# Kernel optimization log

Hardware: AMD Instinct MI355X
Metric: run time of the kernel (lower is better)

The kernel has to match this reference:

```python
import jax, jax.numpy as jnp
from jax import lax
import numpy as np

# ---- static config (matches init_kwargs) ----
B, H, W = 8, 32, 32
L = H * W                      # 1024 tokens
D_MODEL = 384
MAMBA_DIM = 192                # d_model * d_mamba_ratio
LOCAL_DIM = 192
D_INNER = 384                  # expand_m * MAMBA_DIM
D_STATE = 16
D_CONV = 4
DT_RANK = 12                   # ceil(MAMBA_DIM / 16)
NDIR = 4                       # h, h_flip, v, v_flip
RED = 48                       # int(D_INNER * 0.125), BiAttn reduce dim
INNER_C = 192                  # LOCAL_DIM * expand_c
K_C = 8                        # local block depthwise kernel size


def setup_inputs() -> dict:
    key = jax.random.key(0)
    ks = jax.random.split(key, 16)
    s = 0.02
    return {
        "x": jax.random.normal(ks[0], (B, L, D_MODEL), jnp.float32),
        "in_proj_w": jax.random.normal(ks[1], (2 * D_INNER, MAMBA_DIM)) * s,
        "A_log": jnp.broadcast_to(jnp.log(jnp.arange(1, D_STATE + 1, dtype=jnp.float32)), (NDIR, D_INNER, D_STATE)) + 0.0,
        "conv_w": jax.random.normal(ks[2], (NDIR, D_INNER, D_CONV)) * 0.2,
        "conv_b": jax.random.normal(ks[3], (NDIR, D_INNER)) * 0.02,
        "xproj_w": jax.random.normal(ks[4], (NDIR, DT_RANK + 2 * D_STATE, D_INNER)) * s,
        "dtproj_w": jax.random.normal(ks[5], (NDIR, D_INNER, DT_RANK)) * (DT_RANK ** -0.5),
        "dtproj_b": jax.random.normal(ks[6], (NDIR, D_INNER)) * 0.5 - 4.0,
        "Dp": jnp.ones((NDIR, D_INNER)),
        "out_proj_w": jax.random.normal(ks[7], (MAMBA_DIM, D_INNER)) * s,
        "attn_ln_g": jnp.ones((D_INNER,)),
        "attn_ln_b": jnp.zeros((D_INNER,)),
        "attn_gr_w": jax.random.normal(ks[8], (RED, D_INNER)) * s,
        "attn_gr_b": jnp.zeros((RED,)),
        "attn_cs_w": jax.random.normal(ks[9], (D_INNER, RED)) * s,
        "attn_cs_b": jnp.zeros((D_INNER,)),
        "pw1_w": jax.random.normal(ks[10], (2 * INNER_C, LOCAL_DIM)) * s,
        "pw1_b": jnp.zeros((2 * INNER_C,)),
        "dw_w": jax.random.normal(ks[11], (INNER_C, K_C)) * 0.2,
        "dw_b": jnp.zeros((INNER_C,)),
        "bn_g": jnp.ones((INNER_C,)),
        "bn_b": jnp.zeros((INNER_C,)),
        "pw2_w": jax.random.normal(ks[12], (LOCAL_DIM, INNER_C)) * s,
        "pw2_b": jnp.zeros((LOCAL_DIM,)),
    }


def _forward(x, in_proj_w, A_log, conv_w, conv_b, xproj_w, dtproj_w, dtproj_b, Dp,
             out_proj_w, attn_ln_g, attn_ln_b, attn_gr_w, attn_gr_b, attn_cs_w, attn_cs_b,
             pw1_w, pw1_b, dw_w, dw_b, bn_g, bn_b, pw2_w, pw2_b):
    mamba_in = x[:, :, :MAMBA_DIM]
    local_in = x[:, :, MAMBA_DIM:]

    # ---------- MultiMamba branch ----------
    xz = jnp.swapaxes(mamba_in @ in_proj_w.T, 1, 2)   # (B, 2*D_INNER, L)

    def to_dir(t, i):
        # reorder channel-last-token axis per scan direction
        if i == 0:
            return t
        if i == 1:
            return jnp.flip(t, -1)
        tv = t.reshape(B, -1, H, W).swapaxes(-1, -2).reshape(B, -1, L)  # column-major scan
        return tv if i == 2 else jnp.flip(tv, -1)

    def from_dir(t, i):
        if i == 0:
            return t
        if i == 1:
            return jnp.flip(t, -1)
        if i == 3:
            t = jnp.flip(t, -1)
        return t.reshape(B, -1, W, H).swapaxes(-1, -2).reshape(B, -1, L)

    def ssm_dir(xzd, i):
        # mamba_inner_fn_no_out_proj: causal dwconv -> silu -> x_proj -> selective scan -> gate
        xp, z = jnp.split(xzd, 2, axis=1)            # (B, D_INNER, L) each
        xpad = jnp.pad(xp, ((0, 0), (0, 0), (D_CONV - 1, 0)))
        u = lax.conv_general_dilated(xpad, conv_w[i][:, None, :], (1,), 'VALID',
                                     dimension_numbers=('NCH', 'OIH', 'NCH'),
                                     feature_group_count=D_INNER)
        u = jax.nn.silu(u + conv_b[i][None, :, None])
        dbl = jnp.einsum('bdl,rd->brl', u, xproj_w[i])
        dt = dbl[:, :DT_RANK]
        Bm = dbl[:, DT_RANK:DT_RANK + D_STATE]
        Cm = dbl[:, DT_RANK + D_STATE:]
        delta = jax.nn.softplus(jnp.einsum('brl,dr->bdl', dt, dtproj_w[i]) + dtproj_b[i][None, :, None])
        A = -jnp.exp(A_log[i])                        # (D_INNER, D_STATE)

        def step(h, inps):
            d_t, B_t, C_t, u_t = inps                 # (B,d),(B,n),(B,n),(B,d)
            h = jnp.exp(d_t[:, :, None] * A) * h + (d_t * u_t)[:, :, None] * B_t[:, None, :]
            return h, jnp.einsum('bdn,bn->bd', h, C_t)

        h0 = jnp.zeros((B, D_INNER, D_STATE), x.dtype)
        _, ys = lax.scan(step, h0, (delta.transpose(2, 0, 1), Bm.transpose(2, 0, 1),
                                    Cm.transpose(2, 0, 1), u.transpose(2, 0, 1)))
        y = ys.transpose(1, 2, 0) + u * Dp[i][:, None]  # (B, D_INNER, L)
        return y * jax.nn.silu(z)

    def biattn(t):                                     # (B, L, D_INNER)
        mu = t.mean(-1, keepdims=True)
        var = ((t - mu) ** 2).mean(-1, keepdims=True)
        tn = (t - mu) / jnp.sqrt(var + 1e-5) * attn_ln_g + attn_ln_b
        g = tn.mean(1, keepdims=True)                  # global pool (B,1,D_INNER)
        g = jax.nn.gelu(g @ attn_gr_w.T + attn_gr_b, approximate=False)
        c = jax.nn.sigmoid(g @ attn_cs_w.T + attn_cs_b)
        return t * c

    acc = jnp.zeros((B, L, D_INNER), x.dtype)
    for i in range(NDIR):                              # fixed small set of directions
        out_i = from_dir(ssm_dir(to_dir(xz, i), i), i)
        acc = acc + biattn(jnp.swapaxes(out_i, 1, 2))
    mamba_out = acc @ out_proj_w.T                     # (B, L, MAMBA_DIM)

    # ---------- Local conv branch ----------
    hch = jnp.einsum('blc,oc->bol', local_in, pw1_w) + pw1_b[None, :, None]
    a, gte = jnp.split(hch, 2, axis=1)
    hch = a * jax.nn.sigmoid(gte)                      # GLU, (B, INNER_C, L)
    pad_l = K_C // 2
    pad_r = K_C // 2 - (K_C + 1) % 2                   # calc_same_padding(8) -> (4, 3)
    hpad = jnp.pad(hch, ((0, 0), (0, 0), (pad_l, pad_r)))
    hch = lax.conv_general_dilated(hpad, dw_w[:, None, :], (1,), 'VALID',
                                   dimension_numbers=('NCH', 'OIH', 'NCH'),
                                   feature_group_count=INNER_C) + dw_b[None, :, None]
    mu = hch.mean((0, 2))                              # BatchNorm1d (training-mode batch stats)
    var = hch.var((0, 2))
    hch = (hch - mu[None, :, None]) / jnp.sqrt(var + 1e-5)[None, :, None] * bn_g[None, :, None] + bn_b[None, :, None]
    hch = hch * jax.nn.sigmoid(hch)                    # Swish
    local_out = jnp.einsum('bcl,oc->blo', hch, pw2_w) + pw2_b

    return jnp.concatenate([mamba_out, local_out], axis=-1)


def reference(x, in_proj_w, A_log, conv_w, conv_b, xproj_w, dtproj_w, dtproj_b, Dp,
              out_proj_w, attn_ln_g, attn_ln_b, attn_gr_w, attn_gr_b, attn_cs_w, attn_cs_b,
              pw1_w, pw1_b, dw_w, dw_b, bn_g, bn_b, pw2_w, pw2_b):
    return _forward(x, in_proj_w, A_log, conv_w, conv_b, xproj_w, dtproj_w, dtproj_b, Dp,
                    out_proj_w, attn_ln_g, attn_ln_b, attn_gr_w, attn_gr_b, attn_cs_w, attn_cs_b,
                    pw1_w, pw1_b, dw_w, dw_b, bn_g, bn_b, pw2_w, pw2_b)
```

## Files before the change

### kernel.cpp

```cpp
#include <hip/hip_runtime.h>
#include <stdint.h>


#define DEV __device__ __forceinline__

typedef __attribute__((ext_vector_type(8))) short short8;
typedef __attribute__((ext_vector_type(4))) short short4v;
typedef __attribute__((ext_vector_type(4))) float f32x4;

DEV float bf(ushort v) { union { uint32_t u; float f; } c; c.u = ((uint32_t)v) << 16; return c.f; }
DEV ushort fbf(float f) {
  union { float f; uint32_t u; } c; c.f = f;
  uint32_t u = c.u;
  return (ushort)((u + 0x7FFFu + ((u >> 16) & 1u)) >> 16);
}

#if __has_builtin(__builtin_amdgcn_exp2f)
DEV float fexp2(float x) { return __builtin_amdgcn_exp2f(x); }
#else
DEV float fexp2(float x) { return __expf(x * 0.6931471805599453f); }
#endif

template<int CTRL>
DEV float rradd(float x) {
  return x + __int_as_float(__builtin_amdgcn_update_dpp(
      0, __float_as_int(x), CTRL, 0xF, 0xF, true));
}

DEV int pmap(int i, int j) {
  if (i == 0) return j;
  if (i == 1) return 1023 - j;
  if (i == 2) return ((j & 31) << 5) | (j >> 5);
  int k = 1023 - j; return ((k & 31) << 5) | (k >> 5);
}

DEV void cvt4(const float* __restrict__ s, ushort* __restrict__ d, int blk, int tid) {
  const int idx = (blk * 256 + tid) * 4;
  float4 v = *(const float4*)(s + idx);
  d[idx] = fbf(v.x); d[idx + 1] = fbf(v.y); d[idx + 2] = fbf(v.z); d[idx + 3] = fbf(v.w);
}

__global__ __launch_bounds__(256) void prep_all(
    const float* __restrict__ x, ushort* __restrict__ xb,
    const float* __restrict__ ipw, ushort* __restrict__ ipwb,
    const float* __restrict__ opw, ushort* __restrict__ opwb,
    const float* __restrict__ pw1w, ushort* __restrict__ pw1wb,
    const float* __restrict__ pw2w, ushort* __restrict__ pw2wb,
    const float* __restrict__ xw, ushort* __restrict__ xwp)
{
  const int bx = blockIdx.x, tid = threadIdx.x;
  if (bx < 3072)      cvt4(x, xb, bx, tid);
  else if (bx < 3216) cvt4(ipw, ipwb, bx - 3072, tid);
  else if (bx < 3288) cvt4(opw, opwb, bx - 3216, tid);
  else if (bx < 3360) cvt4(pw1w, pw1wb, bx - 3288, tid);
  else if (bx < 3396) cvt4(pw2w, pw2wb, bx - 3360, tid);
  else {
    const int row = bx - 3396;
    const int i = row >> 6, nn = row & 63;
    for (int c = tid; c < 384; c += 256)
      xwp[(size_t)row * 384 + c] = (nn < 44) ? fbf(xw[((size_t)i * 44 + nn) * 384 + c]) : (ushort)0;
  }
}

template<bool BF16OUT, bool BIAS>
__global__ __launch_bounds__(256) void gemm_bt(
    const ushort* __restrict__ A, long long sAz, int lda,
    const ushort* __restrict__ Bw, long long sBz,
    const float* __restrict__ bias,
    void* __restrict__ C, long long sCz, int ldc, int coff, int K)
{
  __shared__ ushort As[64][40];
  __shared__ ushort Bs[64][40];
  A += (size_t)blockIdx.z * sAz;
  Bw += (size_t)blockIdx.z * sBz;
  const int tid = threadIdx.x;
  const int m0 = blockIdx.x * 64, n0 = blockIdx.y * 64;
  const int w = tid >> 6, lane = tid & 63, l15 = lane & 15, quad = lane >> 4;
  const int sr = tid >> 2, sc = (tid & 3) * 8;
  f32x4 acc[4] = {};
  for (int k0 = 0; k0 < K; k0 += 32) {
    __syncthreads();
    *(short8*)&As[sr][sc] = *(const short8*)(A + (size_t)(m0 + sr) * lda + k0 + sc);
    *(short8*)&Bs[sr][sc] = *(const short8*)(Bw + (size_t)(n0 + sr) * K + k0 + sc);
    __syncthreads();
    short8 av = *(short8*)&As[w * 16 + l15][quad * 8];
#pragma unroll
    for (int nt = 0; nt < 4; nt++) {
      short8 bv = *(short8*)&Bs[nt * 16 + l15][quad * 8];
      acc[nt] = __builtin_amdgcn_mfma_f32_16x16x32_bf16(av, bv, acc[nt], 0, 0, 0);
    }
  }
  float* cf = (float*)C + (size_t)blockIdx.z * sCz;
  ushort* cb = (ushort*)C + (size_t)blockIdx.z * sCz;
#pragma unroll
  for (int nt = 0; nt < 4; nt++) {
    const int col = n0 + nt * 16 + l15;
    const float bv = BIAS ? bias[col] : 0.f;
#pragma unroll
    for (int r = 0; r < 4; r++) {
      const int row = m0 + w * 16 + quad * 4 + r;
      float v = acc[nt][r] + bv;
      if (BF16OUT) cb[(size_t)row * ldc + coff + col] = fbf(v);
      else         cf[(size_t)row * ldc + coff + col] = v;
    }
  }
}

__global__ __launch_bounds__(256) void gemm_dual(
    const ushort* __restrict__ A0, int lda0, const ushort* __restrict__ B0,
    const float* __restrict__ bias0, void* __restrict__ C0, int ldc0, int coff0, int K0,
    int nt0, int bf0,
    const ushort* __restrict__ A1, int lda1, const ushort* __restrict__ B1,
    const float* __restrict__ bias1, void* __restrict__ C1, int ldc1, int coff1, int K1,
    int bf1)
{
  __shared__ ushort As[64][40];
  __shared__ ushort Bs[64][40];
  const ushort* A; const ushort* Bw; const float* bias; void* C;
  int lda, ldc, coff, K, bf16o, n0;
  if ((int)blockIdx.y < nt0) {
    A = A0; lda = lda0; Bw = B0; bias = bias0; C = C0; ldc = ldc0; coff = coff0; K = K0;
    bf16o = bf0; n0 = blockIdx.y * 64;
  } else {
    A = A1; lda = lda1; Bw = B1; bias = bias1; C = C1; ldc = ldc1; coff = coff1; K = K1;
    bf16o = bf1; n0 = (blockIdx.y - nt0) * 64;
  }
  const int tid = threadIdx.x;
  const int m0 = blockIdx.x * 64;
  const int w = tid >> 6, lane = tid & 63, l15 = lane & 15, quad = lane >> 4;
  const int sr = tid >> 2, sc = (tid & 3) * 8;
  f32x4 acc[4] = {};
  for (int k0 = 0; k0 < K; k0 += 32) {
    __syncthreads();
    *(short8*)&As[sr][sc] = *(const short8*)(A + (size_t)(m0 + sr) * lda + k0 + sc);
    *(short8*)&Bs[sr][sc] = *(const short8*)(Bw + (size_t)(n0 + sr) * K + k0 + sc);
    __syncthreads();
    short8 av = *(short8*)&As[w * 16 + l15][quad * 8];
#pragma unroll
    for (int nt = 0; nt < 4; nt++) {
      short8 bv = *(short8*)&Bs[nt * 16 + l15][quad * 8];
      acc[nt] = __builtin_amdgcn_mfma_f32_16x16x32_bf16(av, bv, acc[nt], 0, 0, 0);
    }
  }
#pragma unroll
  for (int nt = 0; nt < 4; nt++) {
    const int col = n0 + nt * 16 + l15;
    const float bv = bias ? bias[col] : 0.f;
#pragma unroll
    for (int r = 0; r < 4; r++) {
      const int row = m0 + w * 16 + quad * 4 + r;
      float v = acc[nt][r] + bv;
      if (bf16o) ((ushort*)C)[(size_t)row * ldc + coff + col] = fbf(v);
      else       ((float*)C)[(size_t)row * ldc + coff + col] = v;
    }
  }
}

__global__ __launch_bounds__(256) void gemm_pw2(
    const float* __restrict__ h2, const float* __restrict__ bnsum,
    const float* __restrict__ bng, const float* __restrict__ bnb,
    const ushort* __restrict__ Bw, const float* __restrict__ bias,
    float* __restrict__ C)
{
  __shared__ ushort As[64][40];
  __shared__ ushort Bs[64][40];
  __shared__ float bsc[192], bsh[192];
  const int tid = threadIdx.x;
  const int m0 = blockIdx.x * 64, n0 = blockIdx.y * 64;
  const int w = tid >> 6, lane = tid & 63, l15 = lane & 15, quad = lane >> 4;
  const int sr = tid >> 2, sc = (tid & 3) * 8;
  for (int cth = tid; cth < 192; cth += 256) {
    float m = bnsum[cth] * (1.f / 8192.f);
    float va = bnsum[192 + cth] * (1.f / 8192.f) - m * m;
    float s = bng[cth] * rsqrtf(va + 1e-5f);
    bsc[cth] = s; bsh[cth] = bnb[cth] - m * s;
  }
  f32x4 acc[4] = {};
  for (int k0 = 0; k0 < 192; k0 += 32) {
    __syncthreads();
    {
      const float* hr = h2 + (size_t)(m0 + sr) * 192 + k0 + sc;
      f32x4 a0 = *(const f32x4*)(hr);
      f32x4 a1 = *(const f32x4*)(hr + 4);
      short8 v;
#pragma unroll
      for (int k = 0; k < 8; k++) {
        const float xx = (k < 4) ? a0[k] : a1[k - 4];
        const float xn = xx * bsc[k0 + sc + k] + bsh[k0 + sc + k];
        v[k] = (short)fbf(xn / (1.f + __expf(-xn)));
      }
      *(short8*)&As[sr][sc] = v;
    }
    *(short8*)&Bs[sr][sc] = *(const short8*)(Bw + (size_t)(n0 + sr) * 192 + k0 + sc);
    __syncthreads();
    short8 av = *(short8*)&As[w * 16 + l15][quad * 8];
#pragma unroll
    for (int nt = 0; nt < 4; nt++) {
      short8 bv = *(short8*)&Bs[nt * 16 + l15][quad * 8];
      acc[nt] = __builtin_amdgcn_mfma_f32_16x16x32_bf16(av, bv, acc[nt], 0, 0, 0);
    }
  }
#pragma unroll
  for (int nt = 0; nt < 4; nt++) {
    const int col = n0 + nt * 16 + l15;
    const float bv = bias[col];
#pragma unroll
    for (int r = 0; r < 4; r++) {
      const int row = m0 + w * 16 + quad * 4 + r;
      C[(size_t)row * 384 + 192 + col] = acc[nt][r] + bv;
    }
  }
}

__global__ __launch_bounds__(384) void conv2_kernel(const ushort* __restrict__ xzb,
    const float* __restrict__ cw, const float* __restrict__ cb, ushort* __restrict__ u)
{
  const int d = threadIdx.x;
  const int jt = blockIdx.x;
  const int b = blockIdx.y, i = blockIdx.z;
  __shared__ ushort sx[35][384];
  const int j0 = jt * 32;
#pragma unroll 5
  for (int r = 0; r < 35; r++) {
    const int jj = j0 - 3 + r;
    sx[r][d] = (jj >= 0) ? xzb[(size_t)((b << 10) + pmap(i, jj)) * 768 + d] : (ushort)0;
  }
  __syncthreads();
  const float w0 = cw[((i * 384 + d) << 2) + 0];
  const float w1 = cw[((i * 384 + d) << 2) + 1];
  const float w2 = cw[((i * 384 + d) << 2) + 2];
  const float w3 = cw[((i * 384 + d) << 2) + 3];
  const float cbv = cb[i * 384 + d];
  ushort* ur = u + ((size_t)((i * 8 + b) << 10) + j0) * 384 + d;
#pragma unroll 4
  for (int q = 0; q < 32; q++) {
    float s = bf(sx[q][d]) * w0 + bf(sx[q + 1][d]) * w1 + bf(sx[q + 2][d]) * w2
            + bf(sx[q + 3][d]) * w3 + cbv;
    ur[(size_t)q * 384] = fbf(s / (1.f + __expf(-s)));
  }
}

#define NCH 16
#define CJ 64
__global__ __launch_bounds__(256, 3) void scan9_kernel(
    const ushort* __restrict__ u,
    const float*  __restrict__ dbl,
    const ushort* __restrict__ xzb,
    const float* __restrict__ alog, const float* __restrict__ dtw,
    const float* __restrict__ dtb, const float* __restrict__ Dpw,
    ushort* __restrict__ y)
{
  const int dt0 = blockIdx.x * NCH;
  const int b = blockIdx.y, i = blockIdx.z;
  const int tid = threadIdx.x;
  const int ch = tid >> 4, n = tid & 15;
  const int srow = tid >> 2, role = tid & 3;

  __shared__ float sbc[CJ / 2][68];
  __shared__ float sdu[CJ / 2][68];
  __shared__ float sy[CJ][20];
  __shared__ float sDp[NCH];

  float w48[4][12], dtbv4[4];
#pragma unroll
  for (int cc = 0; cc < 4; cc++) {
    const int chp = 4 * role + cc;
#pragma unroll
    for (int r = 0; r < 12; r++) w48[cc][r] = dtw[((size_t)i * 384 + dt0 + chp) * 12 + r];
    dtbv4[cc] = dtb[i * 384 + dt0 + chp];
  }
  const float L2E = 1.4426950408889634f;
  const float Al = -__expf(alog[((size_t)i * 384 + dt0 + ch) * 16 + n]) * L2E;
  if (tid < NCH) sDp[tid] = Dpw[i * 384 + dt0 + tid];

  const float selm[4] = { (n >> 2) == 0 ? 1.f : 0.f, (n >> 2) == 1 ? 1.f : 0.f,
                          (n >> 2) == 2 ? 1.f : 0.f, (n >> 2) == 3 ? 1.f : 0.f };

  const size_t rb = (size_t)(i * 8 + b) << 10;
  const ushort* ub = u + rb * 384 + dt0;
  const float* dblb = dbl + rb * 64;
  const ushort* zb = xzb + ((size_t)b << 10) * 768 + 384 + dt0;
  ushort* yb = y + rb * 384 + dt0;
  const float* sdup = &sdu[0][4 * ch];
  const float* sbcp = &sbc[0][4 * n];

  f32x4 nd0, nd1, nd2, ns0, ns1, ns2; short4v nu, nz;
  {
    const float* src = dblb + (size_t)srow * 64;
    nd0 = *(const f32x4*)(src); nd1 = *(const f32x4*)(src + 4); nd2 = *(const f32x4*)(src + 8);
    const float* seg = src + role * 12;
    ns0 = *(const f32x4*)(seg); ns1 = *(const f32x4*)(seg + 4); ns2 = *(const f32x4*)(seg + 8);
    nu = *(const short4v*)(ub + (size_t)srow * 384 + 4 * role);
    nz = *(const short4v*)(zb + (size_t)pmap(i, srow) * 768 + 4 * role);
  }

  float h = 0.f;

  for (int c = 0; c < 16; c++) {
    const int j0 = c * CJ;
    f32x4 uf, zf;
#pragma unroll
    for (int k = 0; k < 4; k++) { uf[k] = bf((ushort)nu[k]); zf[k] = bf((ushort)nz[k]); }
    if (role != 0) {
      float vals[12];
#pragma unroll
      for (int k = 0; k < 4; k++) { vals[k] = ns0[k]; vals[4 + k] = ns1[k]; vals[8 + k] = ns2[k]; }
#pragma unroll
      for (int k = 0; k < 12; k++) {
        const int f = role * 12 + k;
        if (f < 44) {
          const int isC = (f >= 28) ? 1 : 0;
          const int nn = isC ? (f - 28) : (f - 12);
          sbc[srow >> 1][4 * nn + 2 * (srow & 1) + isC] = vals[k];
        }
      }
    }
    {
      float dtr[12];
#pragma unroll
      for (int k = 0; k < 4; k++) { dtr[k] = nd0[k]; dtr[4 + k] = nd1[k]; dtr[8 + k] = nd2[k]; }
#pragma unroll
      for (int cc = 0; cc < 4; cc++) {
        float s = dtbv4[cc];
#pragma unroll
        for (int r = 0; r < 12; r++) s += dtr[r] * w48[cc][r];
        const float dl = fmaxf(s, 0.f) + __logf(1.f + __expf(-fabsf(s)));
        float2 pr; pr.x = dl; pr.y = dl * uf[cc];
        *(float2*)&sdu[srow >> 1][4 * (4 * role + cc) + 2 * (srow & 1)] = pr;
      }
    }
    __syncthreads();
    {
      const int cn = (c < 15) ? (c + 1) : 0;
      const int rown = cn * CJ + srow;
      const float* src = dblb + (size_t)rown * 64;
      nd0 = *(const f32x4*)(src); nd1 = *(const f32x4*)(src + 4); nd2 = *(const f32x4*)(src + 8);
      const float* seg = src + role * 12;
      ns0 = *(const f32x4*)(seg); ns1 = *(const f32x4*)(seg + 4); ns2 = *(const f32x4*)(seg + 8);
      nu = *(const short4v*)(ub + (size_t)rown * 384 + 4 * role);
      nz = *(const short4v*)(zb + (size_t)pmap(i, rown) * 768 + 4 * role);
    }
#pragma unroll
    for (int q = 0; q < 4; q++) {
      f32x4 pq = {0.f, 0.f, 0.f, 0.f};
#pragma unroll
      for (int s2 = 0; s2 < 8; s2++) {
        const f32x4 duP = *(const f32x4*)(sdup + (q * 8 + s2) * 68);
        const f32x4 bcP = *(const f32x4*)(sbcp + (q * 8 + s2) * 68);
        {
          const float e = fexp2(duP[0] * Al);
          h = e * h + duP[1] * bcP[0];
          float p = h * bcP[1];
          p = rradd<0x124>(p); p = rradd<0x128>(p);
          pq[s2 >> 1] = fmaf(selm[(2 * s2) & 3], p, pq[s2 >> 1]);
        }
        {
          const float e = fexp2(duP[2] * Al);
          h = e * h + duP[3] * bcP[2];
          float p = h * bcP[3];
          p = rradd<0x124>(p); p = rradd<0x128>(p);
          pq[s2 >> 1] = fmaf(selm[(2 * s2 + 1) & 3], p, pq[s2 >> 1]);
        }
      }
#pragma unroll
      for (int j = 0; j < 4; j++) {
        float t2 = rradd<0xB1>(pq[j]);
        t2 = rradd<0x4E>(t2);
        if ((n & 3) == 0) sy[(q << 4) | (j << 2) | (n >> 2)][ch] = t2;
      }
    }
    __syncthreads();
    {
      const int lo = pmap(i, j0 + srow);
      const f32x4 y4 = *(const f32x4*)&sy[srow][role * 4];
      short4v o;
#pragma unroll
      for (int t = 0; t < 4; t++) {
        const float z = zf[t];
        const float val = (y4[t] + uf[t] * sDp[role * 4 + t]) * (z / (1.f + __expf(-z)));
        o[t] = (short)fbf(val);
      }
      *(short4v*)(yb + (size_t)lo * 384 + role * 4) = o;
    }
  }
}

__global__ __launch_bounds__(256) void lngm_kernel(const ushort* __restrict__ y,
                                                   float* __restrict__ G16)
{
  const int slab = blockIdx.x, b = blockIdx.y, i = blockIdx.z;
  const int tid = threadIdx.x;
  const int w = tid >> 6, lane = tid & 63;
  __shared__ float smu[64], srs[64];
  const size_t base = (size_t)i * 8192 + b * 1024 + slab * 64;
  for (int rr = 0; rr < 16; rr++) {
    const int r = w * 16 + rr;
    const ushort* yr = y + (base + r) * 384;
    float s = 0.f, ss = 0.f;
    const short4v v4 = *(const short4v*)(yr + 4 * lane);
    const uint32_t v2 = *(const uint32_t*)(yr + 256 + 2 * lane);
#pragma unroll
    for (int t = 0; t < 4; t++) { float v = bf((ushort)v4[t]); s += v; ss += v * v; }
    { float v = bf((ushort)(v2 & 0xffffu)); s += v; ss += v * v; }
    { float v = bf((ushort)(v2 >> 16));     s += v; ss += v * v; }
#pragma unroll
    for (int off = 1; off < 64; off <<= 1) { s += __shfl_xor(s, off, 64); ss += __shfl_xor(ss, off, 64); }
    if (lane == 0) {
      float m = s * (1.f / 384.f);
      float va = ss * (1.f / 384.f) - m * m;
      smu[r] = m;
      srs[r] = rsqrtf(va + 1e-5f);
    }
  }
  __syncthreads();
  for (int col = tid; col < 384; col += 256) {
    float s = 0.f;
    for (int r = 0; r < 64; r++)
      s += (bf(y[(base + r) * 384 + col]) - smu[r]) * srs[r];
    G16[((size_t)(i * 8 + b) * 16 + slab) * 384 + col] = s;
  }
}

__global__ __launch_bounds__(64) void gate_kernel(const float* __restrict__ G16,
    const float* __restrict__ lng, const float* __restrict__ lnb,
    const float* __restrict__ grw, const float* __restrict__ grb,
    const float* __restrict__ csw, const float* __restrict__ csb, float* __restrict__ cbuf)
{
  const int b = blockIdx.x, i = blockIdx.y;
  const int ib = i * 8 + b;
  const int lane = threadIdx.x;
  __shared__ float sG[384];
  __shared__ float g48[48];
  for (int dd = lane; dd < 384; dd += 64) {
    const float* g = G16 + (size_t)ib * 16 * 384 + dd;
    float s = 0.f;
#pragma unroll
    for (int k = 0; k < 16; k++) s += g[k * 384];
    sG[dd] = s * (1.f / 1024.f) * lng[dd] + lnb[dd];
  }
  __syncthreads();
  if (lane < 48) {
    float s = grb[lane];
    for (int dd = 0; dd < 384; dd++) s += sG[dd] * grw[lane * 384 + dd];
    g48[lane] = 0.5f * s * (1.f + erff(s * 0.70710678118f));
  }
  __syncthreads();
  for (int dd = lane; dd < 384; dd += 64) {
    float s = csb[dd];
#pragma unroll
    for (int r = 0; r < 48; r++) s += g48[r] * csw[dd * 48 + r];
    cbuf[(size_t)ib * 384 + dd] = 1.f / (1.f + __expf(-s));
  }
}

__global__ __launch_bounds__(384) void accgate_kernel(const ushort* __restrict__ y,
    const float* __restrict__ cbuf, ushort* __restrict__ accb)
{
  const int t = threadIdx.x;
  const int row = blockIdx.x * 4 + (t / 96);
  const int cg = (t % 96) * 4;
  const int b = row >> 10;
  f32x4 s = {};
#pragma unroll
  for (int i = 0; i < 4; i++) {
    const short4v v = *(const short4v*)(y + ((size_t)i * 8192 + row) * 384 + cg);
    const f32x4 cv = *(const f32x4*)(cbuf + (size_t)(i * 8 + b) * 384 + cg);
#pragma unroll
    for (int k = 0; k < 4; k++) s[k] += bf((ushort)v[k]) * cv[k];
  }
  short4v o;
#pragma unroll
  for (int k = 0; k < 4; k++) o[k] = (short)fbf(s[k]);
  *(short4v*)(accb + (size_t)row * 384 + cg) = o;
}

__global__ __launch_bounds__(192) void gludwbn_kernel(const ushort* __restrict__ hchb,
    const float* __restrict__ dww, const float* __restrict__ dwb,
    float* __restrict__ h2, float* __restrict__ bnsum)
{
  const int c = threadIdx.x;
  const int lt = blockIdx.x, b = blockIdx.y;
  __shared__ float sv[39][192];
  const int l0 = lt * 32;
#pragma unroll 4
  for (int r = 0; r < 39; r++) {
    const int ls = l0 + r - 4;
    float v = 0.f;
    if (ls >= 0 && ls < 1024) {
      const size_t rr = (size_t)((b << 10) + ls) * 384;
      const float a = bf(hchb[rr + c]);
      const float g = bf(hchb[rr + 192 + c]);
      v = a / (1.f + __expf(-g));
    }
    sv[r][c] = v;
  }
  __syncthreads();
  float wk[8];
#pragma unroll
  for (int k = 0; k < 8; k++) wk[k] = dww[(c << 3) + k];
  const float bias = dwb[c];
  float sacc = 0.f, ssacc = 0.f;
  for (int q = 0; q < 32; q++) {
    float s = bias;
#pragma unroll
    for (int k = 0; k < 8; k++) s += sv[q + k][c] * wk[k];
    h2[(size_t)((b << 10) + l0 + q) * 192 + c] = s;
    sacc += s; ssacc += s * s;
  }
  atomicAdd(&bnsum[c], sacc);
  atomicAdd(&bnsum[192 + c], ssacc);
}

extern "C" void kernel_launch(void* const* d_in, const int* in_sizes, int n_in,
                              void* d_out, int out_size, void* d_ws, size_t ws_size,
                              hipStream_t stream) {
  const float* x    = (const float*)d_in[0];
  const float* ipw  = (const float*)d_in[1];
  const float* alog = (const float*)d_in[2];
  const float* cw   = (const float*)d_in[3];
  const float* cbv  = (const float*)d_in[4];
  const float* xw   = (const float*)d_in[5];
  const float* dtw  = (const float*)d_in[6];
  const float* dtb  = (const float*)d_in[7];
  const float* Dpw  = (const float*)d_in[8];
  const float* opw  = (const float*)d_in[9];
  const float* lng  = (const float*)d_in[10];
  const float* lnb  = (const float*)d_in[11];
  const float* grw  = (const float*)d_in[12];
  const float* grb  = (const float*)d_in[13];
  const float* csw  = (const float*)d_in[14];
  const float* csb  = (const float*)d_in[15];
  const float* pw1w = (const float*)d_in[16];
  const float* pw1b = (const float*)d_in[17];
  const float* dww  = (const float*)d_in[18];
  const float* dwb  = (const float*)d_in[19];
  const float* bng  = (const float*)d_in[20];
  const float* bnb  = (const float*)d_in[21];
  const float* pw2w = (const float*)d_in[22];
  const float* pw2b = (const float*)d_in[23];
  float* out = (float*)d_out;

  char* ws = (char*)d_ws;
  ushort* xb    = (ushort*)(ws + 0);
  ushort* xzb   = (ushort*)(ws + 6291456);
  ushort* u     = (ushort*)(ws + 18874368);
  float*  dbl   = (float*)(ws + 44040192);
  ushort* y     = (ushort*)(ws + 52428800);
  ushort* accb  = (ushort*)(ws + 77594624);
  float*  G16   = (float*)(ws + 83886080);
  float*  cbuf  = (float*)(ws + 84672512);
  ushort* xwp   = (ushort*)(ws + 84721664);
  ushort* ipwb  = (ushort*)(ws + 84918272);
  ushort* opwb  = (ushort*)(ws + 85213184);
  ushort* pw1wb = (ushort*)(ws + 85360640);
  ushort* pw2wb = (ushort*)(ws + 85508096);
  float*  bnsum = (float*)(ws + 85581824);
  ushort* hchb = (ushort*)(ws + 18874368);
  float*  h2   = (float*)(ws + 34603008);

  prep_all<<<dim3(3652), 256, 0, stream>>>(x, xb, ipw, ipwb, opw, opwb,
                                           pw1w, pw1wb, pw2w, pw2wb, xw, xwp);
  gemm_bt<true, false><<<dim3(128, 12, 1), 256, 0, stream>>>(
      xb, 0, 384, ipwb, 0, nullptr, xzb, 0, 768, 0, 192);
  conv2_kernel<<<dim3(32, 8, 4), 384, 0, stream>>>(xzb, cw, cbv, u);
  gemm_bt<false, false><<<dim3(128, 1, 4), 256, 0, stream>>>(
      u, 8192LL * 384, 384, xwp, 64LL * 384, nullptr, dbl, 8192LL * 64, 64, 0, 384);
  scan9_kernel<<<dim3(24, 8, 4), 256, 0, stream>>>(u, dbl, xzb, alog, dtw, dtb, Dpw, y);
  lngm_kernel<<<dim3(16, 8, 4), 256, 0, stream>>>(y, G16);
  gate_kernel<<<dim3(8, 4), 64, 0, stream>>>(G16, lng, lnb, grw, grb, csw, csb, cbuf);
  accgate_kernel<<<dim3(2048), 384, 0, stream>>>(y, cbuf, accb);
  gemm_dual<<<dim3(128, 9), 256, 0, stream>>>(
      accb, 384, opwb, nullptr, out, 384, 0, 384, 3, 0,
      xb + 192, 384, pw1wb, pw1b, hchb, 384, 0, 192, 1);
  (void)hipMemsetAsync(bnsum, 0, 384 * sizeof(float), stream);
  gludwbn_kernel<<<dim3(32, 8), 192, 0, stream>>>(hchb, dww, dwb, h2, bnsum);
  gemm_pw2<<<dim3(128, 3), 256, 0, stream>>>(h2, bnsum, bng, bnb, pw2wb, pw2b, out);
}
```

Baseline: 324.3 us.

## Write transposed B/C from x-proj GEMM and stream them directly in scan

A dedicated GEMM now writes the dt-rank part into a compact buffer and the B/C state projections transposed (state-major, token-contiguous). The scan kernel loads B and C straight from global memory into registers with double-buffered prefetch, instead of staging them through shared memory. This removes the shared-memory scatter and its bank traffic and shrinks shared usage. The depthwise conv/BN kernel is also split into smaller token tiles to launch more blocks. The trade-off is more global loads per thread and higher register pressure in the scan.

```diff
diff --git a/kernel.cpp b/kernel.cpp
--- a/kernel.cpp
+++ b/kernel.cpp
@@ -103,6 +103,47 @@
       if (BF16OUT) cb[(size_t)row * ldc + coff + col] = fbf(v);
       else         cf[(size_t)row * ldc + coff + col] = v;
     }
+  }
+}
+
+__global__ __launch_bounds__(256) void gemm_dbl(
+    const ushort* __restrict__ A, const ushort* __restrict__ Bw,
+    float* __restrict__ dtbuf, float* __restrict__ dblT)
+{
+  __shared__ ushort As[64][40];
+  __shared__ ushort Bs[64][40];
+  const int z = blockIdx.z;
+  A += (size_t)z * 8192 * 384;
+  Bw += (size_t)z * 64 * 384;
+  const int tid = threadIdx.x;
+  const int m0 = blockIdx.x * 64;
+  const int w = tid >> 6, lane = tid & 63, l15 = lane & 15, quad = lane >> 4;
+  const int sr = tid >> 2, sc = (tid & 3) * 8;
+  f32x4 acc[4] = {};
+  for (int k0 = 0; k0 < 384; k0 += 32) {
+    __syncthreads();
+    *(short8*)&As[sr][sc] = *(const short8*)(A + (size_t)(m0 + sr) * 384 + k0 + sc);
+    *(short8*)&Bs[sr][sc] = *(const short8*)(Bw + (size_t)sr * 384 + k0 + sc);
+    __syncthreads();
+    short8 av = *(short8*)&As[w * 16 + l15][quad * 8];
+#pragma unroll
+    for (int nt = 0; nt < 4; nt++) {
+      short8 bv = *(short8*)&Bs[nt * 16 + l15][quad * 8];
+      acc[nt] = __builtin_amdgcn_mfma_f32_16x16x32_bf16(av, bv, acc[nt], 0, 0, 0);
+    }
+  }
+  const int row0 = m0 + w * 16 + quad * 4;
+#pragma unroll
+  for (int nt = 0; nt < 4; nt++) {
+    const int col = nt * 16 + l15;
+    if (nt == 0) {
+#pragma unroll
+      for (int r = 0; r < 4; r++)
+        dtbuf[((size_t)z * 8192 + row0 + r) * 16 + col] = acc[0][r];
+    }
+    const int tc = col - 12;
+    if (tc >= 0 && tc < 32)
+      *(f32x4*)(dblT + ((size_t)z * 32 + tc) * 8192 + row0) = acc[nt];
   }
 }
 
@@ -242,9 +283,10 @@
 
 #define NCH 16
 #define CJ 64
-__global__ __launch_bounds__(256, 3) void scan9_kernel(
+__global__ __launch_bounds__(256, 3) void scan10_kernel(
     const ushort* __restrict__ u,
-    const float*  __restrict__ dbl,
+    const float*  __restrict__ dtbuf,
+    const float*  __restrict__ dblT,
     const ushort* __restrict__ xzb,
     const float* __restrict__ alog, const float* __restrict__ dtw,
     const float* __restrict__ dtb, const float* __restrict__ Dpw,
@@ -256,8 +298,8 @@
   const int ch = tid >> 4, n = tid & 15;
   const int srow = tid >> 2, role = tid & 3;
 
-  __shared__ float sbc[CJ / 2][68];
-  __shared__ float sdu[CJ / 2][68];
+  __shared__ float sdl[NCH][68];
+  __shared__ float sdlu[NCH][68];
   __shared__ float sy[CJ][20];
   __shared__ float sDp[NCH];
 
@@ -278,43 +320,59 @@
 
   const size_t rb = (size_t)(i * 8 + b) << 10;
   const ushort* ub = u + rb * 384 + dt0;
-  const float* dblb = dbl + rb * 64;
   const ushort* zb = xzb + ((size_t)b << 10) * 768 + 384 + dt0;
   ushort* yb = y + rb * 384 + dt0;
-  const float* sdup = &sdu[0][4 * ch];
-  const float* sbcp = &sbc[0][4 * n];
-
-  f32x4 nd0, nd1, nd2, ns0, ns1, ns2; short4v nu, nz;
+  const float* dtbase = dtbuf + ((size_t)i * 8192 + (b << 10)) * 16;
+  const float* BT = dblT + ((size_t)i * 32 + n) * 8192 + (b << 10);
+  const float* CT = BT + (size_t)16 * 8192;
+
+  f32x4 nd0, nd1, nd2; short4v nu, nz;
   {
-    const float* src = dblb + (size_t)srow * 64;
+    const float* src = dtbase + (size_t)srow * 16;
     nd0 = *(const f32x4*)(src); nd1 = *(const f32x4*)(src + 4); nd2 = *(const f32x4*)(src + 8);
-    const float* seg = src + role * 12;
-    ns0 = *(const f32x4*)(seg); ns1 = *(const f32x4*)(seg + 4); ns2 = *(const f32x4*)(seg + 8);
     nu = *(const short4v*)(ub + (size_t)srow * 384 + 4 * role);
     nz = *(const short4v*)(zb + (size_t)pmap(i, srow) * 768 + 4 * role);
   }
 
   float h = 0.f;
 
+#define QSTEP(Bc, Cc, Bn, Cn, q)                                              \
+    {                                                                         \
+      if ((q) < 3) {                                                          \
+        _Pragma("unroll") for (int g = 0; g < 4; g++) {                       \
+          Bn[g] = *(const f32x4*)(BT + j0 + 16 * ((q) + 1) + 4 * g);          \
+          Cn[g] = *(const f32x4*)(CT + j0 + 16 * ((q) + 1) + 4 * g);          \
+        }                                                                     \
+      }                                                                       \
+      f32x4 pq = {0.f, 0.f, 0.f, 0.f};                                        \
+      _Pragma("unroll") for (int g = 0; g < 4; g++) {                         \
+        const f32x4 dl4 = *(const f32x4*)&sdl[ch][16 * (q) + 4 * g];          \
+        const f32x4 du4 = *(const f32x4*)&sdlu[ch][16 * (q) + 4 * g];         \
+        _Pragma("unroll") for (int t = 0; t < 4; t++) {                       \
+          const float e = fexp2(dl4[t] * Al);                                 \
+          h = e * h + du4[t] * Bc[g][t];                                      \
+          float p = h * Cc[g][t];                                             \
+          p = rradd<0x124>(p); p = rradd<0x128>(p);                           \
+          pq[g] = fmaf(selm[t], p, pq[g]);                                    \
+        }                                                                     \
+      }                                                                       \
+      _Pragma("unroll") for (int g = 0; g < 4; g++) {                         \
+        float t2 = rradd<0xB1>(pq[g]); t2 = rradd<0x4E>(t2);                  \
+        if ((n & 3) == 0) sy[((q) << 4) | (g << 2) | (n >> 2)][ch] = t2;      \
+      }                                                                       \
+    }
+
   for (int c = 0; c < 16; c++) {
     const int j0 = c * CJ;
+    f32x4 BA[4], CA[4], BB[4], CB[4];
+#pragma unroll
+    for (int g = 0; g < 4; g++) {
+      BA[g] = *(const f32x4*)(BT + j0 + 4 * g);
+      CA[g] = *(const f32x4*)(CT + j0 + 4 * g);
+    }
     f32x4 uf, zf;
 #pragma unroll
     for (int k = 0; k < 4; k++) { uf[k] = bf((ushort)nu[k]); zf[k] = bf((ushort)nz[k]); }
-    if (role != 0) {
-      float vals[12];
-#pragma unroll
-      for (int k = 0; k < 4; k++) { vals[k] = ns0[k]; vals[4 + k] = ns1[k]; vals[8 + k] = ns2[k]; }
-#pragma unroll
-      for (int k = 0; k < 12; k++) {
-        const int f = role * 12 + k;
-        if (f < 44) {
-          const int isC = (f >= 28) ? 1 : 0;
-          const int nn = isC ? (f - 28) : (f - 12);
-          sbc[srow >> 1][4 * nn + 2 * (srow & 1) + isC] = vals[k];
-        }
-      }
-    }
     {
       float dtr[12];
 #pragma unroll
@@ -325,50 +383,23 @@
 #pragma unroll
         for (int r = 0; r < 12; r++) s += dtr[r] * w48[cc][r];
         const float dl = fmaxf(s, 0.f) + __logf(1.f + __expf(-fabsf(s)));
-        float2 pr; pr.x = dl; pr.y = dl * uf[cc];
-        *(float2*)&sdu[srow >> 1][4 * (4 * role + cc) + 2 * (srow & 1)] = pr;
+        sdl[4 * role + cc][srow] = dl;
+        sdlu[4 * role + cc][srow] = dl * uf[cc];
       }
     }
     __syncthreads();
     {
       const int cn = (c < 15) ? (c + 1) : 0;
       const int rown = cn * CJ + srow;
-      const float* src = dblb + (size_t)rown * 64;
+      const float* src = dtbase + (size_t)rown * 16;
       nd0 = *(const f32x4*)(src); nd1 = *(const f32x4*)(src + 4); nd2 = *(const f32x4*)(src + 8);
-      const float* seg = src + role * 12;
-      ns0 = *(const f32x4*)(seg); ns1 = *(const f32x4*)(seg + 4); ns2 = *(const f32x4*)(seg + 8);
       nu = *(const short4v*)(ub + (size_t)rown * 384 + 4 * role);
       nz = *(const short4v*)(zb + (size_t)pmap(i, rown) * 768 + 4 * role);
     }
-#pragma unroll
-    for (int q = 0; q < 4; q++) {
-      f32x4 pq = {0.f, 0.f, 0.f, 0.f};
-#pragma unroll
-      for (int s2 = 0; s2 < 8; s2++) {
-        const f32x4 duP = *(const f32x4*)(sdup + (q * 8 + s2) * 68);
-        const f32x4 bcP = *(const f32x4*)(sbcp + (q * 8 + s2) * 68);
-        {
-          const float e = fexp2(duP[0] * Al);
-          h = e * h + duP[1] * bcP[0];
-          float p = h * bcP[1];
-          p = rradd<0x124>(p); p = rradd<0x128>(p);
-          pq[s2 >> 1] = fmaf(selm[(2 * s2) & 3], p, pq[s2 >> 1]);
-        }
-        {
-          const float e = fexp2(duP[2] * Al);
-          h = e * h + duP[3] * bcP[2];
-          float p = h * bcP[3];
-          p = rradd<0x124>(p); p = rradd<0x128>(p);
-          pq[s2 >> 1] = fmaf(selm[(2 * s2 + 1) & 3], p, pq[s2 >> 1]);
-        }
-      }
-#pragma unroll
-      for (int j = 0; j < 4; j++) {
-        float t2 = rradd<0xB1>(pq[j]);
-        t2 = rradd<0x4E>(t2);
-        if ((n & 3) == 0) sy[(q << 4) | (j << 2) | (n >> 2)][ch] = t2;
-      }
-    }
+    QSTEP(BA, CA, BB, CB, 0)
+    QSTEP(BB, CB, BA, CA, 1)
+    QSTEP(BA, CA, BB, CB, 2)
+    QSTEP(BB, CB, BA, CA, 3)
     __syncthreads();
     {
       const int lo = pmap(i, j0 + srow);
@@ -383,6 +414,7 @@
       *(short4v*)(yb + (size_t)lo * 384 + role * 4) = o;
     }
   }
+#undef QSTEP
 }
 
 __global__ __launch_bounds__(256) void lngm_kernel(const ushort* __restrict__ y,
@@ -480,10 +512,10 @@
 {
   const int c = threadIdx.x;
   const int lt = blockIdx.x, b = blockIdx.y;
-  __shared__ float sv[39][192];
-  const int l0 = lt * 32;
+  __shared__ float sv[23][192];
+  const int l0 = lt * 16;
 #pragma unroll 4
-  for (int r = 0; r < 39; r++) {
+  for (int r = 0; r < 23; r++) {
     const int ls = l0 + r - 4;
     float v = 0.f;
     if (ls >= 0 && ls < 1024) {
@@ -500,7 +532,7 @@
   for (int k = 0; k < 8; k++) wk[k] = dww[(c << 3) + k];
   const float bias = dwb[c];
   float sacc = 0.f, ssacc = 0.f;
-  for (int q = 0; q < 32; q++) {
+  for (int q = 0; q < 16; q++) {
     float s = bias;
 #pragma unroll
     for (int k = 0; k < 8; k++) s += sv[q + k][c] * wk[k];
@@ -544,7 +576,8 @@
   ushort* xb    = (ushort*)(ws + 0);
   ushort* xzb   = (ushort*)(ws + 6291456);
   ushort* u     = (ushort*)(ws + 18874368);
-  float*  dbl   = (float*)(ws + 44040192);
+  float*  dtbuf = (float*)(ws + 44040192);
+  float*  dblT  = (float*)(ws + 46137344);
   ushort* y     = (ushort*)(ws + 52428800);
   ushort* accb  = (ushort*)(ws + 77594624);
   float*  G16   = (float*)(ws + 83886080);
@@ -563,9 +596,9 @@
   gemm_bt<true, false><<<dim3(128, 12, 1), 256, 0, stream>>>(
       xb, 0, 384, ipwb, 0, nullptr, xzb, 0, 768, 0, 192);
   conv2_kernel<<<dim3(32, 8, 4), 384, 0, stream>>>(xzb, cw, cbv, u);
-  gemm_bt<false, false><<<dim3(128, 1, 4), 256, 0, stream>>>(
-      u, 8192LL * 384, 384, xwp, 64LL * 384, nullptr, dbl, 8192LL * 64, 64, 0, 384);
-  scan9_kernel<<<dim3(24, 8, 4), 256, 0, stream>>>(u, dbl, xzb, alog, dtw, dtb, Dpw, y);
+  gemm_dbl<<<dim3(128, 1, 4), 256, 0, stream>>>(u, xwp, dtbuf, dblT);
+  scan10_kernel<<<dim3(24, 8, 4), 256, 0, stream>>>(u, dtbuf, dblT, xzb,
+                                                    alog, dtw, dtb, Dpw, y);
   lngm_kernel<<<dim3(16, 8, 4), 256, 0, stream>>>(y, G16);
   gate_kernel<<<dim3(8, 4), 64, 0, stream>>>(G16, lng, lnb, grw, grb, csw, csb, cbuf);
   accgate_kernel<<<dim3(2048), 384, 0, stream>>>(y, cbuf, accb);
@@ -573,6 +606,6 @@
       accb, 384, opwb, nullptr, out, 384, 0, 384, 3, 0,
       xb + 192, 384, pw1wb, pw1b, hchb, 384, 0, 192, 1);
   (void)hipMemsetAsync(bnsum, 0, 384 * sizeof(float), stream);
-  gludwbn_kernel<<<dim3(32, 8), 192, 0, stream>>>(hchb, dww, dwb, h2, bnsum);
+  gludwbn_kernel<<<dim3(64, 8), 192, 0, stream>>>(hchb, dww, dwb, h2, bnsum);
   gemm_pw2<<<dim3(128, 3), 256, 0, stream>>>(h2, bnsum, bng, bnb, pw2wb, pw2b, out);
 }
```

Result: slower. 482.4 us (+48.7%).
